# Performance work log

Measured on AMD Instinct MI355X. Metric: run time of the kernel, lower is better.

The kernel has to match this reference:

```python
import jax, jax.numpy as jnp
from jax import lax
import numpy as np

B, S, D_IN, D_H, D_OUT, FUTURE = 64, 512, 1024, 2048, 1024, 16


def setup_inputs() -> dict:
    key = jax.random.key(0)
    k1, k2, k3 = jax.random.split(key, 3)
    x = jax.random.normal(k1, (B, S, D_IN), dtype=jnp.float32)
    # nn.Linear(input+hidden -> hidden): y = z @ Wh + bh (Wh stores W^T layout)
    Wh = jax.random.normal(k2, (D_IN + D_H, D_H), dtype=jnp.float32) * 0.02
    bh = jnp.zeros((D_H,), dtype=jnp.float32)
    Wo = jax.random.normal(k3, (D_H, D_OUT), dtype=jnp.float32) * 0.02
    bo = jnp.zeros((D_OUT,), dtype=jnp.float32)
    return {"x": x, "Wh": Wh, "bh": bh, "Wo": Wo, "bo": bo, "future": FUTURE}


def reference(x, Wh, bh, Wo, bo, future):
    batch, seq_len, _ = x.shape
    hidden_dim = Wh.shape[1]

    def cell(h, inp):
        # concat + linear + tanh, exactly RnnCell.forward
        combined = jnp.concatenate([inp, h], axis=1)  # [B, D_in + D_h]
        return jnp.tanh(combined @ Wh + bh)

    def step(h, xt):
        h = cell(h, xt)
        return h, h @ Wo + bo

    h0 = jnp.zeros((batch, hidden_dim), dtype=x.dtype)
    # scan over time: xs shaped [S, B, D_in]
    h_last, outs = lax.scan(step, h0, jnp.swapaxes(x, 0, 1))
    output = jnp.swapaxes(outs, 0, 1)  # [B, S, D_out]

    def fstep(carry, _):
        h, inp = carry
        h = cell(h, inp)
        out = h @ Wo + bo
        return (h, out), out  # feed output back as next input

    if future > 0:
        _, pouts = lax.scan(fstep, (h_last, x[:, -1, :]), None, length=future)
        predict = jnp.swapaxes(pouts, 0, 1)  # [B, future, D_out]
    else:
        predict = jnp.zeros((batch, 0, Wo.shape[1]), dtype=x.dtype)
    return output, predict
```

## Files before the change

kernel.cpp:

```cpp
#include <hip/hip_runtime.h>
#include <hip/hip_bf16.h>
#include <math.h>

#define Bz   64
#define Sz   512
#define DIN  1024
#define DH   2048
#define DOUT 1024
#define FUT  16
#define KTOT (DIN + DH)

typedef __attribute__((ext_vector_type(8))) __bf16 bf16x8;
typedef __attribute__((ext_vector_type(4))) float  f32x4;

union U16x8 { uint4 u; bf16x8 v; };

__device__ __forceinline__ uint4 pack_bf8(float4 a, float4 b) {
  bf16x8 t;
  t[0]=(__bf16)a.x; t[1]=(__bf16)a.y; t[2]=(__bf16)a.z; t[3]=(__bf16)a.w;
  t[4]=(__bf16)b.x; t[5]=(__bf16)b.y; t[6]=(__bf16)b.z; t[7]=(__bf16)b.w;
  U16x8 u; u.v = t; return u.u;
}

__device__ __forceinline__ float fast_tanh(float x) {
  const float e = __builtin_amdgcn_exp2f(2.8853900817779268f * x);
  return 1.0f - 2.0f * __builtin_amdgcn_rcpf(e + 1.0f);
}

__device__ __forceinline__ void gload16(const void* g, void* l) {
  __builtin_amdgcn_global_load_lds(
      (const __attribute__((address_space(1))) unsigned int*)g,
      (__attribute__((address_space(3))) unsigned int*)l, 16, 0, 0);
}

template<bool AF32>
__device__ __forceinline__ void gemm_core(
    const void* __restrict__ Abase, size_t astride,
    const __bf16* __restrict__ Bbase, size_t bstride,
    int K, f32x4 acc[2][2])
{
  __shared__ uint4 Al[2][512];
  __shared__ uint4 Bl[2][512];

  const int tid  = threadIdx.x;
  const int lane = tid & 63;
  const int wave = tid >> 6;
  const int wm = (wave >> 1) << 5;
  const int wn = (wave & 1) << 5;
  const int fr = lane & 15;
  const int fg = lane >> 4;

  const int srow = tid >> 2;
  const int sck  = (tid & 3) << 1;

  const int NK = K >> 6;
  if (NK <= 0) return;

  uint4 ra0, ra1, rb0, rb1;

  auto loadt = [&](int kt) {
    const int kelt = (kt << 6) + (sck << 3);
    if constexpr (AF32) {
      const float* ap = (const float*)Abase + (size_t)srow * astride + kelt;
      float4 a0 = *(const float4*)(ap);
      float4 a1 = *(const float4*)(ap + 4);
      float4 a2 = *(const float4*)(ap + 8);
      float4 a3 = *(const float4*)(ap + 12);
      ra0 = pack_bf8(a0, a1);
      ra1 = pack_bf8(a2, a3);
    } else {
      const __bf16* ap = (const __bf16*)Abase + (size_t)srow * astride + kelt;
      ra0 = *(const uint4*)(ap);
      ra1 = *(const uint4*)(ap + 8);
    }
    const __bf16* bp = Bbase + (size_t)srow * bstride + kelt;
    rb0 = *(const uint4*)(bp);
    rb1 = *(const uint4*)(bp + 8);
  };

  auto storet = [&](int buf) {
    const int x7 = srow & 7;
    Al[buf][srow * 8 + ( sck      ^ x7)] = ra0;
    Al[buf][srow * 8 + ((sck + 1) ^ x7)] = ra1;
    Bl[buf][srow * 8 + ( sck      ^ x7)] = rb0;
    Bl[buf][srow * 8 + ((sck + 1) ^ x7)] = rb1;
  };

  loadt(0);
  storet(0);
  __syncthreads();

  for (int kt = 0; kt < NK; ++kt) {
    const int  cur  = kt & 1;
    const bool more = (kt + 1) < NK;
    if (more) loadt(kt + 1);

    #pragma unroll
    for (int kk = 0; kk < 2; ++kk) {
      bf16x8 af[2], bfrag[2];
      #pragma unroll
      for (int mi = 0; mi < 2; ++mi) {
        const int row = wm + mi * 16 + fr;
        const int ck  = (kk * 4 + fg) ^ (row & 7);
        U16x8 u; u.u = Al[cur][row * 8 + ck]; af[mi] = u.v;
      }
      #pragma unroll
      for (int ni = 0; ni < 2; ++ni) {
        const int row = wn + ni * 16 + fr;
        const int ck  = (kk * 4 + fg) ^ (row & 7);
        U16x8 u; u.u = Bl[cur][row * 8 + ck]; bfrag[ni] = u.v;
      }
      #pragma unroll
      for (int mi = 0; mi < 2; ++mi)
        #pragma unroll
        for (int ni = 0; ni < 2; ++ni)
          acc[mi][ni] = __builtin_amdgcn_mfma_f32_16x16x32_bf16(
              af[mi], bfrag[ni], acc[mi][ni], 0, 0, 0);
    }

    __syncthreads();
    if (more) storet((kt + 1) & 1);
    __syncthreads();
  }
}

#define EPI_SETUP() \
  const int tid = threadIdx.x, lane = tid & 63, wave = tid >> 6; \
  const int wm = (wave >> 1) << 5, wn = (wave & 1) << 5; \
  const int fr = lane & 15, fg = lane >> 4;

__global__ __launch_bounds__(256) void k_transp(const float* __restrict__ W,
                                                __bf16* __restrict__ WT,
                                                int K, int N)
{
  __shared__ float T[64][65];
  const int k0 = blockIdx.x << 6, n0 = blockIdx.y << 6;
  const int c = threadIdx.x & 63, r4 = threadIdx.x >> 6;
  #pragma unroll
  for (int rr = 0; rr < 16; ++rr) {
    const int r = rr * 4 + r4;
    T[r][c] = W[(size_t)(k0 + r) * N + n0 + c];
  }
  __syncthreads();
  #pragma unroll
  for (int rr = 0; rr < 16; ++rr) {
    const int r = rr * 4 + r4;
    WT[(size_t)(n0 + r) * K + k0 + c] = (__bf16)T[c][r];
  }
}

__global__ __launch_bounds__(256) void k_xw128(const float* __restrict__ x,
                                               const __bf16* __restrict__ WhT,
                                               const float* __restrict__ bh,
                                               __bf16* __restrict__ HX)
{
  __shared__ __align__(16) uint4 As[1024];
  __shared__ __align__(16) uint4 Bs[1024];

  const int n0 = blockIdx.x << 7;
  const int m0 = blockIdx.y << 7;
  const int tid = threadIdx.x, lane = tid & 63, w = tid >> 6;
  const int wr = w >> 1, wc = w & 1;
  const int fr = lane & 15, fg = lane >> 4;

  const int sr  = tid >> 3;
  const int sq  = tid & 7;
  const int sq2 = sq ^ (sr & 7);

  f32x4 acc[4][4] = {};

  for (int kt = 0; kt < DIN / 64; ++kt) {
    const int ko = kt << 6;
    #pragma unroll
    for (int j = 0; j < 4; ++j) {
      const float* ap = x + (size_t)(m0 + sr + 32 * j) * DIN + ko + (sq2 << 3);
      float4 a0 = *(const float4*)ap;
      float4 a1 = *(const float4*)(ap + 4);
      As[((sr + 32 * j) << 3) + sq] = pack_bf8(a0, a1);
      gload16(WhT + (size_t)(n0 + sr + 32 * j) * KTOT + ko + (sq2 << 3),
              (char*)Bs + (tid << 4) + (j << 12));
    }
    __syncthreads();
    #pragma unroll
    for (int kk = 0; kk < 2; ++kk) {
      bf16x8 af[4], bf_[4];
      const int kq = (kk << 2) + fg;
      #pragma unroll
      for (int mi = 0; mi < 4; ++mi) {
        const int row = (wr << 6) + (mi << 4) + fr;
        U16x8 u; u.u = As[(row << 3) + (kq ^ (row & 7))]; af[mi] = u.v;
      }
      #pragma unroll
      for (int ni = 0; ni < 4; ++ni) {
        const int row = (wc << 6) + (ni << 4) + fr;
        U16x8 u; u.u = Bs[(row << 3) + (kq ^ (row & 7))]; bf_[ni] = u.v;
      }
      #pragma unroll
      for (int mi = 0; mi < 4; ++mi)
        #pragma unroll
        for (int ni = 0; ni < 4; ++ni)
          acc[mi][ni] = __builtin_amdgcn_mfma_f32_16x16x32_bf16(
              af[mi], bf_[ni], acc[mi][ni], 0, 0, 0);
    }
    __syncthreads();
  }

  #pragma unroll
  for (int ni = 0; ni < 4; ++ni) {
    const int n = n0 + (wc << 6) + (ni << 4) + fr;
    const float bn = bh[n];
    #pragma unroll
    for (int mi = 0; mi < 4; ++mi)
      #pragma unroll
      for (int rr = 0; rr < 4; ++rr) {
        const int gf = m0 + (wr << 6) + (mi << 4) + (fg << 2) + rr;
        const int b = gf >> 9, s = gf & 511;
        HX[((size_t)s * Bz + b) * DH + n] = (__bf16)(acc[mi][ni][rr] + bn);
      }
  }
}

__global__ __launch_bounds__(256) void k_out128(const __bf16* __restrict__ HX,
                                                const __bf16* __restrict__ WoT,
                                                const float* __restrict__ bo,
                                                float* __restrict__ out)
{
  __shared__ __align__(16) uint4 As[1024];
  __shared__ __align__(16) uint4 Bs[1024];

  const int n0 = blockIdx.x << 7;
  const int m0 = blockIdx.y << 7;
  const int tid = threadIdx.x, lane = tid & 63, w = tid >> 6;
  const int wr = w >> 1, wc = w & 1;
  const int fr = lane & 15, fg = lane >> 4;

  const int sr  = tid >> 3;
  const int sq  = tid & 7;
  const int sq2 = sq ^ (sr & 7);

  f32x4 acc[4][4] = {};

  for (int kt = 0; kt < DH / 64; ++kt) {
    const int ko = kt << 6;
    #pragma unroll
    for (int j = 0; j < 4; ++j) {
      gload16(HX + (size_t)(m0 + sr + 32 * j) * DH + ko + (sq2 << 3),
              (char*)As + (tid << 4) + (j << 12));
      gload16(WoT + (size_t)(n0 + sr + 32 * j) * DH + ko + (sq2 << 3),
              (char*)Bs + (tid << 4) + (j << 12));
    }
    __syncthreads();
    #pragma unroll
    for (int kk = 0; kk < 2; ++kk) {
      bf16x8 af[4], bf_[4];
      const int kq = (kk << 2) + fg;
      #pragma unroll
      for (int mi = 0; mi < 4; ++mi) {
        const int row = (wr << 6) + (mi << 4) + fr;
        U16x8 u; u.u = As[(row << 3) + (kq ^ (row & 7))]; af[mi] = u.v;
      }
      #pragma unroll
      for (int ni = 0; ni < 4; ++ni) {
        const int row = (wc << 6) + (ni << 4) + fr;
        U16x8 u; u.u = Bs[(row << 3) + (kq ^ (row & 7))]; bf_[ni] = u.v;
      }
      #pragma unroll
      for (int mi = 0; mi < 4; ++mi)
        #pragma unroll
        for (int ni = 0; ni < 4; ++ni)
          acc[mi][ni] = __builtin_amdgcn_mfma_f32_16x16x32_bf16(
              af[mi], bf_[ni], acc[mi][ni], 0, 0, 0);
    }
    __syncthreads();
  }

  #pragma unroll
  for (int ni = 0; ni < 4; ++ni) {
    const int n = n0 + (wc << 6) + (ni << 4) + fr;
    const float bn = bo[n];
    #pragma unroll
    for (int mi = 0; mi < 4; ++mi)
      #pragma unroll
      for (int rr = 0; rr < 4; ++rr) {
        const int gf = m0 + (wr << 6) + (mi << 4) + (fg << 2) + rr;
        const int s = gf >> 6, b = gf & 63;
        out[((size_t)b * Sz + s) * DOUT + n] = acc[mi][ni][rr] + bn;
      }
  }
}

__global__ __launch_bounds__(512, 2) void k_rnn(const __bf16* __restrict__ WhT,
                                                __bf16* __restrict__ HX,
                                                unsigned int* __restrict__ flags)
{
  __shared__ __align__(16) float RED[8 * 1056];

  const int mb    = blockIdx.x & 3;
  const int nb    = blockIdx.x >> 2;
  const int nbase = nb << 6;
  const int tid   = threadIdx.x;
  const int lane  = tid & 63;
  const int w     = tid >> 6;
  const int l15   = lane & 15;
  const int l4    = lane >> 4;
  const int wavek = w << 8;

  bf16x8 wf[8][4];
  {
    const __bf16* wb = WhT + (size_t)(nbase + l15) * KTOT + DIN + wavek + (l4 << 3);
    #pragma unroll
    for (int kk = 0; kk < 8; ++kk)
      #pragma unroll
      for (int nt = 0; nt < 4; ++nt)
        wf[kk][nt] = *(const bf16x8*)(wb + (size_t)nt * 16 * KTOT + kk * 32);
  }

  const int orow = tid >> 5;
  const int cp   = tid & 31;
  const int grow = (mb << 4) + orow;
  const int gcol = nbase + (cp << 1);

  for (int t = 0; t < Sz; ++t) {
    __bf16* Hc = HX + (size_t)t * Bz * DH;

    unsigned int xwp;
    asm volatile("global_load_dword %0, %1, off sc0 sc1"
                 : "=v"(xwp)
                 : "v"((const void*)(Hc + (size_t)grow * DH + gcol))
                 : "memory");

    f32x4 acc[4] = {};

    if (t > 0) {
      const unsigned int* fl = flags
          + (((size_t)(t - 1) * 4 + mb) << 7) + (((w << 2) + (lane & 3)) << 2);
      for (;;) {
        unsigned int f;
        asm volatile("global_load_dword %0, %1, off sc0 sc1\n\t"
                     "s_waitcnt vmcnt(0)"
                     : "=v"(f) : "v"((const void*)fl) : "memory");
        if (__all((int)(f == 1u))) break;
        __builtin_amdgcn_s_sleep(1);
      }

      const __bf16* Hp = HX + (size_t)(t - 1) * Bz * DH
                       + (size_t)((mb << 4) + l15) * DH + wavek + (l4 << 3);
      bf16x8 a[8];
      #pragma unroll
      for (int kk = 0; kk < 8; ++kk)
        a[kk] = *(const bf16x8*)(Hp + kk * 32);

      #pragma unroll
      for (int kk = 0; kk < 8; ++kk)
        #pragma unroll
        for (int nt = 0; nt < 4; ++nt)
          asm("v_mfma_f32_16x16x32_bf16 %0, %1, %2, %0"
              : "+v"(acc[nt]) : "v"(a[kk]), "a"(wf[kk][nt]));
    }

    #pragma unroll
    for (int nt = 0; nt < 4; ++nt)
      #pragma unroll
      for (int r = 0; r < 4; ++r)
        RED[w * 1056 + ((l4 << 2) + r) * 66 + (nt << 4) + l15] = acc[nt][r];
    __syncthreads();

    float sx = 0.f, sy = 0.f;
    #pragma unroll
    for (int p = 0; p < 8; ++p) {
      const float2 v = *(const float2*)&RED[p * 1056 + orow * 66 + (cp << 1)];
      sx += v.x; sy += v.y;
    }

    asm volatile("s_waitcnt vmcnt(0)" : "+v"(xwp) :: "memory");
    union { unsigned int u; __bf16 h[2]; } ux; ux.u = xwp;
    union { unsigned int u; __bf16 h[2]; } po;
    po.h[0] = (__bf16)fast_tanh(sx + (float)ux.h[0]);
    po.h[1] = (__bf16)fast_tanh(sy + (float)ux.h[1]);

    asm volatile("global_store_dword %0, %1, off sc0 sc1"
                 :: "v"((void*)(Hc + (size_t)grow * DH + gcol)), "v"(po.u)
                 : "memory");
    asm volatile("s_waitcnt vmcnt(0)" ::: "memory");
    __syncthreads();
    if (tid == 0) {
      unsigned int* fp = flags + (((size_t)t * 4 + mb) << 7) + (nb << 2);
      asm volatile("global_store_dword %0, %1, off sc0 sc1"
                   :: "v"((void*)fp), "v"(1u) : "memory");
    }
  }
}

__global__ __launch_bounds__(256) void k_finit(const float* __restrict__ x,
                                               const __bf16* __restrict__ HX,
                                               __bf16* __restrict__ zf0)
{
  const int b = blockIdx.x;
  for (int k = threadIdx.x; k < DIN; k += 256)
    zf0[(size_t)b * KTOT + k] =
        (__bf16)x[((size_t)b * Sz + (Sz - 1)) * DIN + k];
  for (int k = threadIdx.x; k < DH; k += 256)
    zf0[(size_t)b * KTOT + DIN + k] =
        HX[(size_t)(Sz - 1) * Bz * DH + (size_t)b * DH + k];
}

__global__ __launch_bounds__(256) void k_fstep(const __bf16* __restrict__ zc,
                                               __bf16* __restrict__ zn,
                                               const __bf16* __restrict__ WhT,
                                               const float* __restrict__ bh)
{
  const int n0 = blockIdx.x << 6;
  f32x4 acc[2][2] = {};
  gemm_core<false>(zc, KTOT, WhT + (size_t)n0 * KTOT, KTOT, KTOT, acc);
  EPI_SETUP();
  #pragma unroll
  for (int mi = 0; mi < 2; ++mi)
    #pragma unroll
    for (int ni = 0; ni < 2; ++ni)
      #pragma unroll
      for (int r = 0; r < 4; ++r) {
        const int m = wm + mi * 16 + fg * 4 + r;
        const int n = n0 + wn + ni * 16 + fr;
        zn[(size_t)m * KTOT + DIN + n] = (__bf16)fast_tanh(acc[mi][ni][r] + bh[n]);
      }
}

__global__ __launch_bounds__(256) void k_fout(__bf16* __restrict__ zn,
                                              const __bf16* __restrict__ WoT,
                                              const float* __restrict__ bo,
                                              float* __restrict__ pred,
                                              int f)
{
  const int n0 = blockIdx.x << 6;
  f32x4 acc[2][2] = {};
  gemm_core<false>(zn + DIN, KTOT, WoT + (size_t)n0 * DH, DH, DH, acc);
  EPI_SETUP();
  #pragma unroll
  for (int mi = 0; mi < 2; ++mi)
    #pragma unroll
    for (int ni = 0; ni < 2; ++ni)
      #pragma unroll
      for (int r = 0; r < 4; ++r) {
        const int m = wm + mi * 16 + fg * 4 + r;
        const int n = n0 + wn + ni * 16 + fr;
        const float v = acc[mi][ni][r] + bo[n];
        pred[((size_t)m * FUT + f) * DOUT + n] = v;
        zn[(size_t)m * KTOT + n] = (__bf16)v;
      }
}

extern "C" void kernel_launch(void* const* d_in, const int* in_sizes, int n_in,
                              void* d_out, int out_size, void* d_ws, size_t ws_size,
                              hipStream_t stream)
{
  const float* x  = (const float*)d_in[0];
  const float* Wh = (const float*)d_in[1];
  const float* bh = (const float*)d_in[2];
  const float* Wo = (const float*)d_in[3];
  const float* bo = (const float*)d_in[4];

  char* ws = (char*)d_ws;
  __bf16* WhT = (__bf16*)ws;
  __bf16* WoT = WhT + (size_t)DH * KTOT;
  __bf16* HX  = WoT + (size_t)DOUT * DH;
  __bf16* zf  = HX + (size_t)Sz * Bz * DH;
  unsigned int* flags = (unsigned int*)(zf + (size_t)2 * Bz * KTOT);

  float* out  = (float*)d_out;
  float* pred = out + (size_t)Bz * Sz * DOUT;

  const dim3 blk(256);

  k_transp<<<dim3(KTOT / 64, DH / 64), blk, 0, stream>>>(Wh, WhT, KTOT, DH);
  k_transp<<<dim3(DH / 64, DOUT / 64), blk, 0, stream>>>(Wo, WoT, DH, DOUT);

  hipMemsetAsync(flags, 0, (size_t)Sz * 4 * 128 * sizeof(unsigned int), stream);

  k_xw128<<<dim3(DH / 128, (Bz * Sz) / 128), blk, 0, stream>>>(x, WhT, bh, HX);

  {
    const __bf16* a0 = WhT; __bf16* a1 = HX; unsigned int* a2 = flags;
    void* args[] = { (void*)&a0, (void*)&a1, (void*)&a2 };
    hipLaunchCooperativeKernel((const void*)k_rnn, dim3(128), dim3(512), args,
                               0, stream);
  }

  k_out128<<<dim3(DOUT / 128, (Bz * Sz) / 128), blk, 0, stream>>>(HX, WoT, bo, out);

  k_finit<<<dim3(Bz), blk, 0, stream>>>(x, HX, zf);
  for (int f = 0; f < FUT; ++f) {
    __bf16* zc = zf + (size_t)(f & 1) * Bz * KTOT;
    __bf16* zn = zf + (size_t)((f & 1) ^ 1) * Bz * KTOT;
    k_fstep<<<dim3(DH / 64), blk, 0, stream>>>(zc, zn, WhT, bh);
    k_fout<<<dim3(DOUT / 64), blk, 0, stream>>>(zn, WoT, bo, pred, f);
  }
}
```

Before: 3.216 ms.

## Fuse future-prediction steps into one persistent cooperative kernel with flag sync

Replaces the 16-step loop of separate hidden-step and output kernel launches with a single cooperative kernel of 48 blocks. 32 blocks compute the hidden update and 16 compute the output projection, synchronised per step through polled global flags. Each step writes to a distinct slot of a staging buffer placed at the start of the HX workspace, so no ping-pong buffer is needed. The aim is to remove the launch overhead and inter-kernel gaps. In exchange it adds spin-polling latency, and the bounded poll loop gives up after a fixed number of tries and proceeds even if the flags are not set.

```diff
diff --git a/kernel.cpp b/kernel.cpp
--- a/kernel.cpp
+++ b/kernel.cpp
@@ -9,6 +9,9 @@
 #define DOUT 1024
 #define FUT  16
 #define KTOT (DIN + DH)
+
+#define FUTF_OFF (Sz * 4 * 128)
+#define FLAG_WORDS (FUTF_OFF + FUT * 48)
 
 typedef __attribute__((ext_vector_type(8))) __bf16 bf16x8;
 typedef __attribute__((ext_vector_type(4))) float  f32x4;
@@ -124,11 +127,6 @@
   }
 }
 
-#define EPI_SETUP() \
-  const int tid = threadIdx.x, lane = tid & 63, wave = tid >> 6; \
-  const int wm = (wave >> 1) << 5, wn = (wave & 1) << 5; \
-  const int fr = lane & 15, fg = lane >> 4;
-
 __global__ __launch_bounds__(256) void k_transp(const float* __restrict__ W,
                                                 __bf16* __restrict__ WT,
                                                 int K, int N)
@@ -393,60 +391,97 @@
 
 __global__ __launch_bounds__(256) void k_finit(const float* __restrict__ x,
                                                const __bf16* __restrict__ HX,
-                                               __bf16* __restrict__ zf0)
+                                               __bf16* __restrict__ zs0)
 {
   const int b = blockIdx.x;
   for (int k = threadIdx.x; k < DIN; k += 256)
-    zf0[(size_t)b * KTOT + k] =
+    zs0[(size_t)b * KTOT + k] =
         (__bf16)x[((size_t)b * Sz + (Sz - 1)) * DIN + k];
   for (int k = threadIdx.x; k < DH; k += 256)
-    zf0[(size_t)b * KTOT + DIN + k] =
+    zs0[(size_t)b * KTOT + DIN + k] =
         HX[(size_t)(Sz - 1) * Bz * DH + (size_t)b * DH + k];
 }
 
-__global__ __launch_bounds__(256) void k_fstep(const __bf16* __restrict__ zc,
-                                               __bf16* __restrict__ zn,
-                                               const __bf16* __restrict__ WhT,
-                                               const float* __restrict__ bh)
-{
-  const int n0 = blockIdx.x << 6;
-  f32x4 acc[2][2] = {};
-  gemm_core<false>(zc, KTOT, WhT + (size_t)n0 * KTOT, KTOT, KTOT, acc);
-  EPI_SETUP();
-  #pragma unroll
-  for (int mi = 0; mi < 2; ++mi)
-    #pragma unroll
-    for (int ni = 0; ni < 2; ++ni)
-      #pragma unroll
-      for (int r = 0; r < 4; ++r) {
-        const int m = wm + mi * 16 + fg * 4 + r;
-        const int n = n0 + wn + ni * 16 + fr;
-        zn[(size_t)m * KTOT + DIN + n] = (__bf16)fast_tanh(acc[mi][ni][r] + bh[n]);
-      }
-}
-
-__global__ __launch_bounds__(256) void k_fout(__bf16* __restrict__ zn,
-                                              const __bf16* __restrict__ WoT,
-                                              const float* __restrict__ bo,
-                                              float* __restrict__ pred,
-                                              int f)
-{
-  const int n0 = blockIdx.x << 6;
-  f32x4 acc[2][2] = {};
-  gemm_core<false>(zn + DIN, KTOT, WoT + (size_t)n0 * DH, DH, DH, acc);
-  EPI_SETUP();
-  #pragma unroll
-  for (int mi = 0; mi < 2; ++mi)
-    #pragma unroll
-    for (int ni = 0; ni < 2; ++ni)
-      #pragma unroll
-      for (int r = 0; r < 4; ++r) {
-        const int m = wm + mi * 16 + fg * 4 + r;
-        const int n = n0 + wn + ni * 16 + fr;
-        const float v = acc[mi][ni][r] + bo[n];
-        pred[((size_t)m * FUT + f) * DOUT + n] = v;
-        zn[(size_t)m * KTOT + n] = (__bf16)v;
-      }
+__global__ __launch_bounds__(256) void k_fut(const __bf16* __restrict__ WhT,
+                                             const __bf16* __restrict__ WoT,
+                                             const float* __restrict__ bh,
+                                             const float* __restrict__ bo,
+                                             __bf16* __restrict__ zs,
+                                             float* __restrict__ pred,
+                                             unsigned int* __restrict__ futf)
+{
+  const int blk   = blockIdx.x;
+  const bool roleA = (blk < 32);
+  const int n0    = (roleA ? blk : blk - 32) << 6;
+
+  const int tid = threadIdx.x, lane = tid & 63, wave = tid >> 6;
+  const int wm = (wave >> 1) << 5, wn = (wave & 1) << 5;
+  const int fr = lane & 15, fg = lane >> 4;
+
+  for (int f = 0; f < FUT; ++f) {
+    const bool needPoll = roleA ? (f > 0) : true;
+    if (needPoll) {
+      const unsigned int* fb = futf + (size_t)(roleA ? f - 1 : f) * 48;
+      const int nflags = roleA ? 48 : 32;
+      const int idx = lane < nflags ? lane : 0;
+      int guard = 0;
+      for (;;) {
+        unsigned int v;
+        asm volatile("global_load_dword %0, %1, off sc0 sc1\n\t"
+                     "s_waitcnt vmcnt(0)"
+                     : "=v"(v) : "v"((const void*)(fb + idx)) : "memory");
+        if (__all((int)(v == 1u))) break;
+        if (++guard > (1 << 15)) break;
+        __builtin_amdgcn_s_sleep(1);
+      }
+    }
+
+    const __bf16* Ab = roleA ? zs + (size_t)f * Bz * KTOT
+                             : zs + (size_t)(f + 1) * Bz * KTOT + DIN;
+    const __bf16* Bb = roleA ? WhT + (size_t)n0 * KTOT
+                             : WoT + (size_t)n0 * DH;
+    const size_t bstr = roleA ? (size_t)KTOT : (size_t)DH;
+    const int    K    = roleA ? KTOT : DH;
+
+    f32x4 acc[2][2] = {};
+    gemm_core<false>(Ab, KTOT, Bb, bstr, K, acc);
+
+    __bf16* zn = zs + (size_t)(f + 1) * Bz * KTOT;
+    #pragma unroll
+    for (int mi = 0; mi < 2; ++mi)
+      #pragma unroll
+      for (int ni = 0; ni < 2; ++ni)
+        #pragma unroll
+        for (int r = 0; r < 4; ++r) {
+          const int m = wm + mi * 16 + fg * 4 + r;
+          const int n = n0 + wn + ni * 16 + fr;
+          if (roleA) {
+            union { __bf16 h; unsigned short us; } cv;
+            cv.h = (__bf16)fast_tanh(acc[mi][ni][r] + bh[n]);
+            const unsigned int val = cv.us;
+            asm volatile("global_store_short %0, %1, off sc0 sc1"
+                         :: "v"((void*)(zn + (size_t)m * KTOT + DIN + n)),
+                            "v"(val) : "memory");
+          } else {
+            const float v = acc[mi][ni][r] + bo[n];
+            pred[((size_t)m * FUT + f) * DOUT + n] = v;
+            union { __bf16 h; unsigned short us; } cv;
+            cv.h = (__bf16)v;
+            const unsigned int val = cv.us;
+            asm volatile("global_store_short %0, %1, off sc0 sc1"
+                         :: "v"((void*)(zn + (size_t)m * KTOT + n)),
+                            "v"(val) : "memory");
+          }
+        }
+
+    asm volatile("s_waitcnt vmcnt(0)" ::: "memory");
+    __syncthreads();
+    if (tid == 0) {
+      unsigned int* fp = futf + (size_t)f * 48 + blk;
+      asm volatile("global_store_dword %0, %1, off sc0 sc1"
+                   :: "v"((void*)fp), "v"(1u) : "memory");
+    }
+  }
 }
 
 extern "C" void kernel_launch(void* const* d_in, const int* in_sizes, int n_in,
@@ -463,8 +498,8 @@
   __bf16* WhT = (__bf16*)ws;
   __bf16* WoT = WhT + (size_t)DH * KTOT;
   __bf16* HX  = WoT + (size_t)DOUT * DH;
-  __bf16* zf  = HX + (size_t)Sz * Bz * DH;
-  unsigned int* flags = (unsigned int*)(zf + (size_t)2 * Bz * KTOT);
+  unsigned int* flags = (unsigned int*)(HX + (size_t)Sz * Bz * DH);
+  __bf16* zs = HX;
 
   float* out  = (float*)d_out;
   float* pred = out + (size_t)Bz * Sz * DOUT;
@@ -474,7 +509,7 @@
   k_transp<<<dim3(KTOT / 64, DH / 64), blk, 0, stream>>>(Wh, WhT, KTOT, DH);
   k_transp<<<dim3(DH / 64, DOUT / 64), blk, 0, stream>>>(Wo, WoT, DH, DOUT);
 
-  hipMemsetAsync(flags, 0, (size_t)Sz * 4 * 128 * sizeof(unsigned int), stream);
+  hipMemsetAsync(flags, 0, (size_t)FLAG_WORDS * sizeof(unsigned int), stream);
 
   k_xw128<<<dim3(DH / 128, (Bz * Sz) / 128), blk, 0, stream>>>(x, WhT, bh, HX);
 
@@ -487,11 +522,16 @@
 
   k_out128<<<dim3(DOUT / 128, (Bz * Sz) / 128), blk, 0, stream>>>(HX, WoT, bo, out);
 
-  k_finit<<<dim3(Bz), blk, 0, stream>>>(x, HX, zf);
-  for (int f = 0; f < FUT; ++f) {
-    __bf16* zc = zf + (size_t)(f & 1) * Bz * KTOT;
-    __bf16* zn = zf + (size_t)((f & 1) ^ 1) * Bz * KTOT;
-    k_fstep<<<dim3(DH / 64), blk, 0, stream>>>(zc, zn, WhT, bh);
-    k_fout<<<dim3(DOUT / 64), blk, 0, stream>>>(zn, WoT, bo, pred, f);
-  }
-}
+  k_finit<<<dim3(Bz), blk, 0, stream>>>(x, HX, zs);
+
+  {
+    const __bf16* a0 = WhT; const __bf16* a1 = WoT;
+    const float* a2 = bh; const float* a3 = bo;
+    __bf16* a4 = zs; float* a5 = pred;
+    unsigned int* a6 = flags + FUTF_OFF;
+    void* args[] = { (void*)&a0, (void*)&a1, (void*)&a2, (void*)&a3,
+                     (void*)&a4, (void*)&a5, (void*)&a6 };
+    hipLaunchCooperativeKernel((const void*)k_fut, dim3(48), blk, args,
+                               0, stream);
+  }
+}
```

Result: slower. 3.382 ms (+5.2%).

## Fold output projection into recurrent weights for future steps and batch prediction GEMM

Applied to the files above, without the earlier changes.

Precomputes a combined weight Wc = Wo·Wh_in + Wh_h and bias bc = bh + bo·Wh_in, so each future step needs only one 2048-wide GEMM on the hidden state instead of a hidden GEMM plus an output GEMM. All future hidden states are stored, and the predictions are computed afterward in a single batched GEMM over 16×64 rows. This removes 15 small kernel launches and their serial dependence, at the cost of a one-time 2048×2048×1024 weight-combining GEMM. Reusing the HX buffer region as scratch after it has been consumed, and rounding the folded weights to bf16, adds some numeric risk.

```diff
diff --git a/kernel.cpp b/kernel.cpp
--- a/kernel.cpp
+++ b/kernel.cpp
@@ -33,10 +33,10 @@
       (__attribute__((address_space(3))) unsigned int*)l, 16, 0, 0);
 }
 
-template<bool AF32>
+template<bool AF32, bool BF32>
 __device__ __forceinline__ void gemm_core(
     const void* __restrict__ Abase, size_t astride,
-    const __bf16* __restrict__ Bbase, size_t bstride,
+    const void* __restrict__ Bbase, size_t bstride,
     int K, f32x4 acc[2][2])
 {
   __shared__ uint4 Al[2][512];
@@ -73,9 +73,19 @@
       ra0 = *(const uint4*)(ap);
       ra1 = *(const uint4*)(ap + 8);
     }
-    const __bf16* bp = Bbase + (size_t)srow * bstride + kelt;
-    rb0 = *(const uint4*)(bp);
-    rb1 = *(const uint4*)(bp + 8);
+    if constexpr (BF32) {
+      const float* bp = (const float*)Bbase + (size_t)srow * bstride + kelt;
+      float4 b0 = *(const float4*)(bp);
+      float4 b1 = *(const float4*)(bp + 4);
+      float4 b2 = *(const float4*)(bp + 8);
+      float4 b3 = *(const float4*)(bp + 12);
+      rb0 = pack_bf8(b0, b1);
+      rb1 = pack_bf8(b2, b3);
+    } else {
+      const __bf16* bp = (const __bf16*)Bbase + (size_t)srow * bstride + kelt;
+      rb0 = *(const uint4*)(bp);
+      rb1 = *(const uint4*)(bp + 8);
+    }
   };
 
   auto storet = [&](int buf) {
@@ -391,16 +401,54 @@
   }
 }
 
+__global__ __launch_bounds__(256) void k_wcomb(const __bf16* __restrict__ WhT,
+                                               const float* __restrict__ Wo,
+                                               __bf16* __restrict__ WcT)
+{
+  const int k0 = blockIdx.x << 6;
+  const int n0 = blockIdx.y << 6;
+  f32x4 acc[2][2] = {};
+  gemm_core<false, true>(WhT + (size_t)n0 * KTOT, KTOT,
+                         Wo + (size_t)k0 * DOUT, DOUT, DIN, acc);
+  EPI_SETUP();
+  #pragma unroll
+  for (int mi = 0; mi < 2; ++mi)
+    #pragma unroll
+    for (int ni = 0; ni < 2; ++ni)
+      #pragma unroll
+      for (int r = 0; r < 4; ++r) {
+        const int n = n0 + wm + mi * 16 + fg * 4 + r;
+        const int k = k0 + wn + ni * 16 + fr;
+        WcT[(size_t)n * DH + k] =
+            (__bf16)(acc[mi][ni][r] + (float)WhT[(size_t)n * KTOT + DIN + k]);
+      }
+}
+
+__global__ __launch_bounds__(256) void k_bc(const float* __restrict__ bh,
+                                            const float* __restrict__ bo,
+                                            const __bf16* __restrict__ WhT,
+                                            float* __restrict__ bc)
+{
+  const int lane = threadIdx.x & 63;
+  const int n = blockIdx.x * 4 + (threadIdx.x >> 6);
+  float s = 0.f;
+  for (int j0 = 0; j0 < DIN; j0 += 64)
+    s += bo[j0 + lane] * (float)WhT[(size_t)n * KTOT + j0 + lane];
+  #pragma unroll
+  for (int off = 32; off; off >>= 1) s += __shfl_down(s, off);
+  if (lane == 0) bc[n] = bh[n] + s;
+}
+
 __global__ __launch_bounds__(256) void k_finit(const float* __restrict__ x,
                                                const __bf16* __restrict__ HX,
-                                               __bf16* __restrict__ zf0)
+                                               __bf16* __restrict__ zs0)
 {
   const int b = blockIdx.x;
   for (int k = threadIdx.x; k < DIN; k += 256)
-    zf0[(size_t)b * KTOT + k] =
+    zs0[(size_t)b * KTOT + k] =
         (__bf16)x[((size_t)b * Sz + (Sz - 1)) * DIN + k];
   for (int k = threadIdx.x; k < DH; k += 256)
-    zf0[(size_t)b * KTOT + DIN + k] =
+    zs0[(size_t)b * KTOT + DIN + k] =
         HX[(size_t)(Sz - 1) * Bz * DH + (size_t)b * DH + k];
 }
 
@@ -411,7 +459,7 @@
 {
   const int n0 = blockIdx.x << 6;
   f32x4 acc[2][2] = {};
-  gemm_core<false>(zc, KTOT, WhT + (size_t)n0 * KTOT, KTOT, KTOT, acc);
+  gemm_core<false, false>(zc, KTOT, WhT + (size_t)n0 * KTOT, KTOT, KTOT, acc);
   EPI_SETUP();
   #pragma unroll
   for (int mi = 0; mi < 2; ++mi)
@@ -425,15 +473,14 @@
       }
 }
 
-__global__ __launch_bounds__(256) void k_fout(__bf16* __restrict__ zn,
-                                              const __bf16* __restrict__ WoT,
-                                              const float* __restrict__ bo,
-                                              float* __restrict__ pred,
-                                              int f)
+__global__ __launch_bounds__(256) void k_fstepc(const __bf16* __restrict__ gh,
+                                                __bf16* __restrict__ zn,
+                                                const __bf16* __restrict__ WcT,
+                                                const float* __restrict__ bc)
 {
   const int n0 = blockIdx.x << 6;
   f32x4 acc[2][2] = {};
-  gemm_core<false>(zn + DIN, KTOT, WoT + (size_t)n0 * DH, DH, DH, acc);
+  gemm_core<false, false>(gh, KTOT, WcT + (size_t)n0 * DH, DH, DH, acc);
   EPI_SETUP();
   #pragma unroll
   for (int mi = 0; mi < 2; ++mi)
@@ -443,9 +490,31 @@
       for (int r = 0; r < 4; ++r) {
         const int m = wm + mi * 16 + fg * 4 + r;
         const int n = n0 + wn + ni * 16 + fr;
-        const float v = acc[mi][ni][r] + bo[n];
-        pred[((size_t)m * FUT + f) * DOUT + n] = v;
-        zn[(size_t)m * KTOT + n] = (__bf16)v;
+        zn[(size_t)m * KTOT + DIN + n] = (__bf16)fast_tanh(acc[mi][ni][r] + bc[n]);
+      }
+}
+
+__global__ __launch_bounds__(256) void k_predb(const __bf16* __restrict__ zs,
+                                               const __bf16* __restrict__ WoT,
+                                               const float* __restrict__ bo,
+                                               float* __restrict__ pred)
+{
+  const int n0 = blockIdx.x << 6;
+  const int m0 = blockIdx.y << 6;
+  f32x4 acc[2][2] = {};
+  gemm_core<false, false>(zs + (size_t)(64 + m0) * KTOT + DIN, KTOT,
+                          WoT + (size_t)n0 * DH, DH, DH, acc);
+  EPI_SETUP();
+  #pragma unroll
+  for (int mi = 0; mi < 2; ++mi)
+    #pragma unroll
+    for (int ni = 0; ni < 2; ++ni)
+      #pragma unroll
+      for (int r = 0; r < 4; ++r) {
+        const int m = m0 + wm + mi * 16 + fg * 4 + r;
+        const int n = n0 + wn + ni * 16 + fr;
+        const int f = m >> 6, b = m & 63;
+        pred[((size_t)b * FUT + f) * DOUT + n] = acc[mi][ni][r] + bo[n];
       }
 }
 
@@ -463,8 +532,12 @@
   __bf16* WhT = (__bf16*)ws;
   __bf16* WoT = WhT + (size_t)DH * KTOT;
   __bf16* HX  = WoT + (size_t)DOUT * DH;
-  __bf16* zf  = HX + (size_t)Sz * Bz * DH;
-  unsigned int* flags = (unsigned int*)(zf + (size_t)2 * Bz * KTOT);
+  unsigned int* flags = (unsigned int*)(HX + (size_t)Sz * Bz * DH);
+
+  char* hb = (char*)HX;
+  __bf16* WcT = (__bf16*)hb;
+  float*  bc  = (float*)(hb + (8u << 20));
+  __bf16* zs  = (__bf16*)(hb + (9u << 20));
 
   float* out  = (float*)d_out;
   float* pred = out + (size_t)Bz * Sz * DOUT;
@@ -487,11 +560,15 @@
 
   k_out128<<<dim3(DOUT / 128, (Bz * Sz) / 128), blk, 0, stream>>>(HX, WoT, bo, out);
 
-  k_finit<<<dim3(Bz), blk, 0, stream>>>(x, HX, zf);
-  for (int f = 0; f < FUT; ++f) {
-    __bf16* zc = zf + (size_t)(f & 1) * Bz * KTOT;
-    __bf16* zn = zf + (size_t)((f & 1) ^ 1) * Bz * KTOT;
-    k_fstep<<<dim3(DH / 64), blk, 0, stream>>>(zc, zn, WhT, bh);
-    k_fout<<<dim3(DOUT / 64), blk, 0, stream>>>(zn, WoT, bo, pred, f);
-  }
-}
+  k_finit<<<dim3(Bz), blk, 0, stream>>>(x, HX, zs);
+  k_wcomb<<<dim3(DH / 64, DH / 64), blk, 0, stream>>>(WhT, Wo, WcT);
+  k_bc<<<dim3(DH / 4), blk, 0, stream>>>(bh, bo, WhT, bc);
+
+  k_fstep<<<dim3(DH / 64), blk, 0, stream>>>(zs, zs + (size_t)Bz * KTOT, WhT, bh);
+  for (int f = 1; f < FUT; ++f) {
+    const __bf16* gh = zs + (size_t)f * Bz * KTOT + DIN;
+    __bf16*       zn = zs + (size_t)(f + 1) * Bz * KTOT;
+    k_fstepc<<<dim3(DH / 64), blk, 0, stream>>>(gh, zn, WcT, bc);
+  }
+  k_predb<<<dim3(DOUT / 64, (FUT * Bz) / 64), blk, 0, stream>>>(zs, WoT, bo, pred);
+}
```

Result: faster. 2.928 ms (-8.9%).
